# Performance work log

Hardware: AMD Instinct MI355X
Metric: run time of the kernel (lower is better)

Reference implementation:

```python
import jax, jax.numpy as jnp
import numpy as np

KERNEL_MUL = 2.0
KERNEL_NUM = 5


def setup_inputs() -> dict:
    key = jax.random.key(0)
    k1, k2 = jax.random.split(key)
    source = jax.random.normal(k1, (4096, 512), dtype=jnp.float32)
    target = jax.random.normal(k2, (4096, 512), dtype=jnp.float32)
    return {"source": source, "target": target}


def reference(source, target):
    B = source.shape[0]
    src = source.reshape(B, -1)
    tgt = target.reshape(B, -1)
    total = jnp.concatenate([src, tgt], axis=0)  # [2B, D]
    n = 2 * B

    # Pairwise squared L2 via ||a||^2 + ||b||^2 - 2 a.b (GEMM trick)
    sq = jnp.sum(total * total, axis=-1)  # [2B]
    d2 = sq[:, None] + sq[None, :] - 2.0 * (total @ total.T)  # [2B, 2B]
    d2 = jnp.maximum(d2, 0.0)

    # Median-heuristic-style bandwidth; torch uses L2_distance.data (no grad)
    bandwidth = jax.lax.stop_gradient(jnp.sum(d2)) / (n * n - n)
    bandwidth = bandwidth / (KERNEL_MUL ** (KERNEL_NUM // 2))

    # Multi-bandwidth Gaussian kernel sum
    kernels = jnp.zeros_like(d2)
    for i in range(KERNEL_NUM):
        kernels = kernels + jnp.exp(-d2 / (bandwidth * (KERNEL_MUL ** i)))

    XX = kernels[:B, :B]
    YY = kernels[B:, B:]
    XY = kernels[:B, B:]
    YX = kernels[B:, :B]
    return jnp.mean(XX + YY - XY - YX)
```

## Files before the change

kernel.cpp:

```cpp
#include <hip/hip_runtime.h>
#include <hip/hip_bf16.h>


typedef int   i32x4 __attribute__((ext_vector_type(4)));
typedef float f32x4 __attribute__((ext_vector_type(4)));

#define N_TOT  8192
#define NHALF  4096
#define DIM    512
#define BM     128
#define TILES  64
#define NPAIRS 2080
#define QSCALE 24.0f
#define IMG_OFF    327680ULL
#define IMG_BYTES  4194304ULL

__device__ __forceinline__ int q8(float x) {
    int q = __float2int_rn(x * QSCALE);
    return max(-127, min(127, q));
}

__global__ __launch_bounds__(256) void k_pre(
    const float* __restrict__ src, const float* __restrict__ tgt,
    unsigned char* __restrict__ img,
    float* __restrict__ sq, float* __restrict__ vp)
{
    __shared__ float tile[64][65];
    __shared__ float vredq[4][512];
    const int b  = blockIdx.x;
    const int p  = b >> 1, hf = b & 1;
    const int t  = threadIdx.x;
    const float* base = ((p < 32) ? src + (size_t)p * BM * DIM
                                  : tgt + (size_t)(p - 32) * BM * DIM)
                        + (size_t)(hf * 64) * DIM;
    const int lrow = t >> 2;
    const int qcs  = (t & 3) * 16;
    float rowsq = 0.f;

    for (int kk = 0; kk < 8; ++kk) {
        const float* qp = base + (size_t)lrow * DIM + kk * 64 + qcs;
        #pragma unroll
        for (int j = 0; j < 4; ++j) {
            float4 x = *(const float4*)(qp + j * 4);
            int q0 = q8(x.x), q1 = q8(x.y), q2 = q8(x.z), q3 = q8(x.w);
            tile[lrow][qcs + j * 4 + 0] = (float)q0;
            tile[lrow][qcs + j * 4 + 1] = (float)q1;
            tile[lrow][qcs + j * 4 + 2] = (float)q2;
            tile[lrow][qcs + j * 4 + 3] = (float)q3;
            rowsq += (float)(q0 * q0 + q1 * q1 + q2 * q2 + q3 * q3);
        }
        __syncthreads();
        {
            int g_l = t >> 6, lane = t & 63;
            int r = g_l * 16 + (lane & 15), c0 = (lane >> 4) * 16;
            unsigned int w[4];
            #pragma unroll
            for (int wi = 0; wi < 4; ++wi) {
                int a0 = (int)tile[r][c0 + wi * 4 + 0];
                int a1 = (int)tile[r][c0 + wi * 4 + 1];
                int a2 = (int)tile[r][c0 + wi * 4 + 2];
                int a3 = (int)tile[r][c0 + wi * 4 + 3];
                w[wi] = (a0 & 255) | ((a1 & 255) << 8) | ((a2 & 255) << 16)
                        | ((unsigned)(a3 & 255) << 24);
            }
            *(uint4*)(img + (size_t)p * 65536 + (size_t)kk * 8192
                      + (size_t)(hf * 4 + g_l) * 1024 + (size_t)lane * 16) =
                make_uint4(w[0], w[1], w[2], w[3]);
        }
        {
            int c = t & 63, rq = t >> 6;
            float s = 0.f;
            #pragma unroll
            for (int r = 0; r < 16; ++r) s += tile[rq * 16 + r][c];
            vredq[rq][kk * 64 + c] = s;
        }
        __syncthreads();
    }
    rowsq += __shfl_xor(rowsq, 1);
    rowsq += __shfl_xor(rowsq, 2);
    if ((t & 3) == 0) sq[p * BM + hf * 64 + lrow] = rowsq;
    vp[(size_t)b * 512 + t]       = vredq[0][t] + vredq[1][t] + vredq[2][t] + vredq[3][t];
    vp[(size_t)b * 512 + t + 256] = vredq[0][t + 256] + vredq[1][t + 256]
                                  + vredq[2][t + 256] + vredq[3][t + 256];
}

__global__ void k3_bw(const float* __restrict__ sq, const float* __restrict__ vp,
                      float* __restrict__ craw) {
    int t = threadIdx.x;
    double s = 0.0;
    for (int i = t; i < N_TOT; i += 512) s += (double)sq[i];
    float vs = 0.f;
    for (int p = 0; p < 128; ++p) vs += vp[(size_t)p * 512 + t];
    double vv = (double)vs * vs;
    #pragma unroll
    for (int off = 32; off > 0; off >>= 1) {
        s  += __shfl_down(s, off);
        vv += __shfl_down(vv, off);
    }
    __shared__ double rs[8], rv[8];
    if ((t & 63) == 0) { rs[t >> 6] = s; rv[t >> 6] = vv; }
    __syncthreads();
    if (t == 0) {
        double S = 0.0, V = 0.0;
        for (int i = 0; i < 8; ++i) { S += rs[i]; V += rv[i]; }
        double sumd2 = 2.0 * (double)N_TOT * S - 2.0 * V;
        double bw = sumd2 / ((double)N_TOT * N_TOT - (double)N_TOT) / 4.0;
        *craw = (float)(1.4426950408889634 / (16.0 * bw));
    }
}

#define LOAD8(A, B, KP)                                              \
    do {                                                             \
        const char* a_ = gA + (size_t)(KP) * 8192;                   \
        const char* b_ = gB + (size_t)(KP) * 8192;                   \
        A[0] = *(const i32x4*)(a_ + vA);                             \
        A[1] = *(const i32x4*)(a_ + vA + 1024);                      \
        A[2] = *(const i32x4*)(a_ + vA + 2048);                      \
        A[3] = *(const i32x4*)(a_ + vA + 3072);                      \
        B[0] = *(const i32x4*)(b_ + vB);                             \
        B[1] = *(const i32x4*)(b_ + vB + 1024);                      \
        B[2] = *(const i32x4*)(b_ + vB + 2048);                      \
        B[3] = *(const i32x4*)(b_ + vB + 3072);                      \
    } while (0)

#define MFMA16(A, B)                                                           \
    do {                                                                       \
        _Pragma("unroll")                                                      \
        for (int m_ = 0; m_ < 4; ++m_)                                         \
            _Pragma("unroll")                                                  \
            for (int n_ = 0; n_ < 4; ++n_)                                     \
                acc[m_][n_] = __builtin_amdgcn_mfma_i32_16x16x64_i8(           \
                    A[m_], B[n_], acc[m_][n_], 0, 0, 0);                       \
    } while (0)

__global__ __launch_bounds__(256) void kmain(
    const unsigned char* __restrict__ img,
    const float* __restrict__ sq, const float* __restrict__ craw_p,
    float* __restrict__ Fpart)
{
    __shared__ float red[4];

    int b = blockIdx.x;
    int s = (b & 7) * (NPAIRS / 8) + (b >> 3);
    int SI = 0, rem = s;
    while (rem >= 10 + 16 * (15 - SI)) { rem -= 10 + 16 * (15 - SI); ++SI; }
    int I, J;
    if (rem < 10) {
        int di = 0;
        while (rem >= 4 - di) { rem -= 4 - di; ++di; }
        I = SI * 4 + di; J = SI * 4 + di + rem;
    } else {
        rem -= 10;
        int SJ = SI + 1 + (rem >> 4);
        I = SI * 4 + ((rem >> 2) & 3);
        J = SJ * 4 + (rem & 3);
    }

    const int tid  = threadIdx.x;
    const int lane = tid & 63;
    const int wid  = tid >> 6;
    const int wr   = wid >> 1, wc = wid & 1;
    const int lhi  = lane >> 4, llo = lane & 15;

    const char* gA = (const char*)img + (size_t)I * 65536;
    const char* gB = (const char*)img + (size_t)J * 65536;
    const int vA = wr * 4096 + lane * 16;
    const int vB = wc * 4096 + lane * 16;

    i32x4 acc[4][4];
    #pragma unroll
    for (int m = 0; m < 4; ++m)
        #pragma unroll
        for (int n = 0; n < 4; ++n) acc[m][n] = (i32x4){0, 0, 0, 0};

    i32x4 a0[4], b0[4], a1[4], b1[4];
    LOAD8(a0, b0, 0);
    #pragma unroll
    for (int kp = 0; kp < 8; kp += 2) {
        LOAD8(a1, b1, kp + 1);
        MFMA16(a0, b0);
        LOAD8(a0, b0, (kp + 2) & 7);
        MFMA16(a1, b1);
    }

    const float c = *craw_p;
    const int rI = I * BM, rJ = J * BM;

    float sqr_[4][4], sqc_[4];
    #pragma unroll
    for (int m = 0; m < 4; ++m)
        #pragma unroll
        for (int r = 0; r < 4; ++r)
            sqr_[m][r] = sq[rI + wr * 64 + m * 16 + lhi * 4 + r];
    #pragma unroll
    for (int n = 0; n < 4; ++n)
        sqc_[n] = sq[rJ + wc * 64 + n * 16 + llo];

    float local = 0.f;
    #pragma unroll
    for (int m = 0; m < 4; ++m)
        #pragma unroll
        for (int n = 0; n < 4; ++n)
            #pragma unroll
            for (int r = 0; r < 4; ++r) {
                float d2 = sqr_[m][r] + sqc_[n] - 2.f * (float)acc[m][n][r];
                d2 = fmaxf(d2, 0.f);
                float u = __builtin_amdgcn_exp2f(-d2 * c);
                float u2 = u * u, u4 = u2 * u2, u8 = u4 * u4, u16 = u8 * u8;
                local += u + u2 + u4 + u8 + u16;
            }

    float wgt = ((I < 32) == (J < 32)) ? 1.f : -1.f;
    if (I != J) wgt *= 2.f;
    local *= wgt;

    #pragma unroll
    for (int off = 32; off > 0; off >>= 1) local += __shfl_down(local, off);
    if (lane == 0) red[wid] = local;
    __syncthreads();
    if (tid == 0) Fpart[b] = red[0] + red[1] + red[2] + red[3];
}

__global__ void k4_out(const float* __restrict__ Fpart, float* __restrict__ out) {
    int t = threadIdx.x;
    double s = 0.0;
    for (int i = t; i < NPAIRS; i += 256) s += (double)Fpart[i];
    #pragma unroll
    for (int off = 32; off > 0; off >>= 1) s += __shfl_down(s, off);
    __shared__ double r[4];
    if ((t & 63) == 0) r[t >> 6] = s;
    __syncthreads();
    if (t == 0) out[0] = (float)((r[0] + r[1] + r[2] + r[3]) / ((double)NHALF * (double)NHALF));
}

extern "C" void kernel_launch(void* const* d_in, const int* in_sizes, int n_in,
                              void* d_out, int out_size, void* d_ws, size_t ws_size,
                              hipStream_t stream) {
    const float* src = (const float*)d_in[0];
    const float* tgt = (const float*)d_in[1];
    char* ws = (char*)d_ws;
    float* sq    = (float*)ws;
    float* vp    = (float*)(ws + 32768);
    float* craw  = (float*)(ws + 294912);
    float* Fpart = (float*)(ws + 295040);
    unsigned char* img = (unsigned char*)(ws + IMG_OFF);
    float* out = (float*)d_out;

    hipLaunchKernelGGL(k_pre, dim3(128), dim3(256), 0, stream, src, tgt, img, sq, vp);
    hipLaunchKernelGGL(k3_bw, dim3(1), dim3(512), 0, stream, sq, vp, craw);
    hipLaunchKernelGGL(kmain, dim3(NPAIRS), dim3(256), 0, stream, img, sq, craw, Fpart);
    hipLaunchKernelGGL(k4_out, dim3(1), dim3(256), 0, stream, Fpart, out);
}
```

Measured before the change: 58.03 us.

## Split quantize prepass across more blocks with atomics; triple-buffer MFMA loads

The quantization prepass now uses 512 blocks, one per row-panel and k-chunk, instead of 128. Each block packs int8 directly into shared memory and accumulates row norms and column sums with atomicAdd into a zeroed workspace. This removes the per-panel partial-vector buffer and shrinks the bandwidth reduction kernel. The main kernel loads the squared norms before the GEMM and uses a three-deep register load pipeline to hide global latency, at the cost of more registers and an extra memset launch.

```diff
diff --git a/kernel.cpp b/kernel.cpp
--- a/kernel.cpp
+++ b/kernel.cpp
@@ -13,7 +13,6 @@
 #define NPAIRS 2080
 #define QSCALE 24.0f
 #define IMG_OFF    327680ULL
-#define IMG_BYTES  4194304ULL
 
 __device__ __forceinline__ int q8(float x) {
     int q = __float2int_rn(x * QSCALE);
@@ -23,86 +22,65 @@
 __global__ __launch_bounds__(256) void k_pre(
     const float* __restrict__ src, const float* __restrict__ tgt,
     unsigned char* __restrict__ img,
-    float* __restrict__ sq, float* __restrict__ vp)
+    float* __restrict__ sq, float* __restrict__ v)
 {
-    __shared__ float tile[64][65];
-    __shared__ float vredq[4][512];
-    const int b  = blockIdx.x;
-    const int p  = b >> 1, hf = b & 1;
-    const int t  = threadIdx.x;
+    __shared__ __align__(16) signed char qt[BM][80];
+    const int b = blockIdx.x;
+    const int p = b >> 3, kp = b & 7;
+    const int t = threadIdx.x;
     const float* base = ((p < 32) ? src + (size_t)p * BM * DIM
-                                  : tgt + (size_t)(p - 32) * BM * DIM)
-                        + (size_t)(hf * 64) * DIM;
-    const int lrow = t >> 2;
-    const int qcs  = (t & 3) * 16;
-    float rowsq = 0.f;
-
-    for (int kk = 0; kk < 8; ++kk) {
-        const float* qp = base + (size_t)lrow * DIM + kk * 64 + qcs;
-        #pragma unroll
-        for (int j = 0; j < 4; ++j) {
+                                  : tgt + (size_t)(p - 32) * BM * DIM) + kp * 64;
+
+    {
+        int r = t >> 1, ch = (t & 1) * 32;
+        const float* qp = base + (size_t)r * DIM + ch;
+        float rsq = 0.f;
+        #pragma unroll
+        for (int j = 0; j < 8; ++j) {
             float4 x = *(const float4*)(qp + j * 4);
             int q0 = q8(x.x), q1 = q8(x.y), q2 = q8(x.z), q3 = q8(x.w);
-            tile[lrow][qcs + j * 4 + 0] = (float)q0;
-            tile[lrow][qcs + j * 4 + 1] = (float)q1;
-            tile[lrow][qcs + j * 4 + 2] = (float)q2;
-            tile[lrow][qcs + j * 4 + 3] = (float)q3;
-            rowsq += (float)(q0 * q0 + q1 * q1 + q2 * q2 + q3 * q3);
+            unsigned int w = (q0 & 255) | ((q1 & 255) << 8) | ((q2 & 255) << 16)
+                             | ((unsigned)(q3 & 255) << 24);
+            *(unsigned int*)&qt[r][ch + j * 4] = w;
+            rsq += (float)(q0 * q0 + q1 * q1 + q2 * q2 + q3 * q3);
         }
-        __syncthreads();
-        {
-            int g_l = t >> 6, lane = t & 63;
-            int r = g_l * 16 + (lane & 15), c0 = (lane >> 4) * 16;
-            unsigned int w[4];
-            #pragma unroll
-            for (int wi = 0; wi < 4; ++wi) {
-                int a0 = (int)tile[r][c0 + wi * 4 + 0];
-                int a1 = (int)tile[r][c0 + wi * 4 + 1];
-                int a2 = (int)tile[r][c0 + wi * 4 + 2];
-                int a3 = (int)tile[r][c0 + wi * 4 + 3];
-                w[wi] = (a0 & 255) | ((a1 & 255) << 8) | ((a2 & 255) << 16)
-                        | ((unsigned)(a3 & 255) << 24);
-            }
-            *(uint4*)(img + (size_t)p * 65536 + (size_t)kk * 8192
-                      + (size_t)(hf * 4 + g_l) * 1024 + (size_t)lane * 16) =
-                make_uint4(w[0], w[1], w[2], w[3]);
-        }
-        {
-            int c = t & 63, rq = t >> 6;
-            float s = 0.f;
-            #pragma unroll
-            for (int r = 0; r < 16; ++r) s += tile[rq * 16 + r][c];
-            vredq[rq][kk * 64 + c] = s;
-        }
-        __syncthreads();
-    }
-    rowsq += __shfl_xor(rowsq, 1);
-    rowsq += __shfl_xor(rowsq, 2);
-    if ((t & 3) == 0) sq[p * BM + hf * 64 + lrow] = rowsq;
-    vp[(size_t)b * 512 + t]       = vredq[0][t] + vredq[1][t] + vredq[2][t] + vredq[3][t];
-    vp[(size_t)b * 512 + t + 256] = vredq[0][t + 256] + vredq[1][t + 256]
-                                  + vredq[2][t + 256] + vredq[3][t + 256];
-}
-
-__global__ void k3_bw(const float* __restrict__ sq, const float* __restrict__ vp,
+        rsq += __shfl_xor(rsq, 1);
+        if ((t & 1) == 0) atomicAdd(&sq[p * BM + r], rsq);
+    }
+    __syncthreads();
+    #pragma unroll
+    for (int h = 0; h < 2; ++h) {
+        int ci = t + h * 256;
+        int g = ci >> 6, lane = ci & 63;
+        int row = g * 16 + (lane & 15), c0 = (lane >> 4) * 16;
+        uint4 w = *(const uint4*)&qt[row][c0];
+        *(uint4*)(img + (size_t)p * 65536 + (size_t)kp * 8192
+                  + (size_t)g * 1024 + (size_t)lane * 16) = w;
+    }
+    if (t < 64) {
+        float s = 0.f;
+        for (int r = 0; r < BM; ++r) s += (float)qt[r][t];
+        atomicAdd(&v[kp * 64 + t], s);
+    }
+}
+
+__global__ void k3_bw(const float* __restrict__ sq, const float* __restrict__ v,
                       float* __restrict__ craw) {
     int t = threadIdx.x;
-    double s = 0.0;
-    for (int i = t; i < N_TOT; i += 512) s += (double)sq[i];
-    float vs = 0.f;
-    for (int p = 0; p < 128; ++p) vs += vp[(size_t)p * 512 + t];
-    double vv = (double)vs * vs;
+    double s = 0.0, vv = 0.0;
+    for (int i = t; i < N_TOT; i += 256) s += (double)sq[i];
+    for (int i = t; i < DIM; i += 256) { double x = (double)v[i]; vv += x * x; }
     #pragma unroll
     for (int off = 32; off > 0; off >>= 1) {
         s  += __shfl_down(s, off);
         vv += __shfl_down(vv, off);
     }
-    __shared__ double rs[8], rv[8];
+    __shared__ double rs[4], rv[4];
     if ((t & 63) == 0) { rs[t >> 6] = s; rv[t >> 6] = vv; }
     __syncthreads();
     if (t == 0) {
-        double S = 0.0, V = 0.0;
-        for (int i = 0; i < 8; ++i) { S += rs[i]; V += rv[i]; }
+        double S = rs[0] + rs[1] + rs[2] + rs[3];
+        double V = rv[0] + rv[1] + rv[2] + rv[3];
         double sumd2 = 2.0 * (double)N_TOT * S - 2.0 * V;
         double bw = sumd2 / ((double)N_TOT * N_TOT - (double)N_TOT) / 4.0;
         *craw = (float)(1.4426950408889634 / (16.0 * bw));
@@ -167,25 +145,8 @@
     const int vA = wr * 4096 + lane * 16;
     const int vB = wc * 4096 + lane * 16;
 
-    i32x4 acc[4][4];
-    #pragma unroll
-    for (int m = 0; m < 4; ++m)
-        #pragma unroll
-        for (int n = 0; n < 4; ++n) acc[m][n] = (i32x4){0, 0, 0, 0};
-
-    i32x4 a0[4], b0[4], a1[4], b1[4];
-    LOAD8(a0, b0, 0);
-    #pragma unroll
-    for (int kp = 0; kp < 8; kp += 2) {
-        LOAD8(a1, b1, kp + 1);
-        MFMA16(a0, b0);
-        LOAD8(a0, b0, (kp + 2) & 7);
-        MFMA16(a1, b1);
-    }
-
     const float c = *craw_p;
     const int rI = I * BM, rJ = J * BM;
-
     float sqr_[4][4], sqc_[4];
     #pragma unroll
     for (int m = 0; m < 4; ++m)
@@ -195,6 +156,25 @@
     #pragma unroll
     for (int n = 0; n < 4; ++n)
         sqc_[n] = sq[rJ + wc * 64 + n * 16 + llo];
+
+    i32x4 acc[4][4];
+    #pragma unroll
+    for (int m = 0; m < 4; ++m)
+        #pragma unroll
+        for (int n = 0; n < 4; ++n) acc[m][n] = (i32x4){0, 0, 0, 0};
+
+    i32x4 aA[4], bA[4], aB[4], bB[4], aC[4], bC[4];
+    LOAD8(aA, bA, 0);
+    LOAD8(aB, bB, 1);
+    LOAD8(aC, bC, 2);
+    MFMA16(aA, bA); LOAD8(aA, bA, 3);
+    MFMA16(aB, bB); LOAD8(aB, bB, 4);
+    MFMA16(aC, bC); LOAD8(aC, bC, 5);
+    MFMA16(aA, bA); LOAD8(aA, bA, 6);
+    MFMA16(aB, bB); LOAD8(aB, bB, 7);
+    MFMA16(aC, bC);
+    MFMA16(aA, bA);
+    MFMA16(aB, bB);
 
     float local = 0.f;
     #pragma unroll
@@ -240,14 +220,15 @@
     const float* tgt = (const float*)d_in[1];
     char* ws = (char*)d_ws;
     float* sq    = (float*)ws;
-    float* vp    = (float*)(ws + 32768);
-    float* craw  = (float*)(ws + 294912);
+    float* v     = (float*)(ws + 32768);
+    float* craw  = (float*)(ws + 34816);
     float* Fpart = (float*)(ws + 295040);
     unsigned char* img = (unsigned char*)(ws + IMG_OFF);
     float* out = (float*)d_out;
 
-    hipLaunchKernelGGL(k_pre, dim3(128), dim3(256), 0, stream, src, tgt, img, sq, vp);
-    hipLaunchKernelGGL(k3_bw, dim3(1), dim3(512), 0, stream, sq, vp, craw);
+    hipMemsetAsync(ws, 0, 34816, stream);
+    hipLaunchKernelGGL(k_pre, dim3(512), dim3(256), 0, stream, src, tgt, img, sq, v);
+    hipLaunchKernelGGL(k3_bw, dim3(1), dim3(256), 0, stream, sq, v, craw);
     hipLaunchKernelGGL(kmain, dim3(NPAIRS), dim3(256), 0, stream, img, sq, craw, Fpart);
     hipLaunchKernelGGL(k4_out, dim3(1), dim3(256), 0, stream, Fpart, out);
 }
```

Measured after the change: 59.48 us. 1.02x slower.
